# Kernel optimization log

Measured on AMD Instinct MI355X. Metric: run time of the kernel, lower is better.

Reference implementation:

```python
import jax, jax.numpy as jnp
import numpy as np

D_MODEL = 1024
D_INNER = 2048      # expand=2
D_STATE = 128
NHEADS = 32
HEADDIM = 64
DCONV = 4
CONV_DIM = D_INNER + 2 * D_STATE                 # x, B, C channels through conv
D_IN_PROJ = 2 * D_INNER + 2 * D_STATE + NHEADS   # z, xBC, dt
NBLOCKS = 4


def _mlp(x, w1, b1, w2, b2):
    # MLP(2, in, out): Linear(in,in) -> ReLU -> Linear(in,out)
    return jax.nn.relu(x @ w1 + b1) @ w2 + b2


def _mamba2_block(u, Wi, cw, cb, dtb, Alog, Dsk, nw, Wo):
    B, L, _ = u.shape
    zxbcdt = u @ Wi                                        # [B,L,D_IN_PROJ]
    z, xBC, dt = jnp.split(zxbcdt, [D_INNER, D_INNER + CONV_DIM], axis=-1)
    # causal depthwise conv1d, kernel 4
    pad = jnp.pad(xBC, ((0, 0), (DCONV - 1, 0), (0, 0)))
    conv = cb
    for k in range(DCONV):
        conv = conv + pad[:, k:k + L, :] * cw[:, k]
    xBC = jax.nn.silu(conv)
    xh, Bm, Cm = jnp.split(xBC, [D_INNER, D_INNER + D_STATE], axis=-1)
    dt = jax.nn.softplus(dt + dtb)                         # [B,L,H]
    A = -jnp.exp(Alog)                                     # [H], negative
    xh = xh.reshape(B, L, NHEADS, HEADDIM)

    def step(h, inp):
        x_t, dt_t, b_t, c_t = inp                          # [B,H,P],[B,H],[B,N],[B,N]
        dA = jnp.exp(dt_t * A)                             # [B,H]
        h = h * dA[..., None, None] + (dt_t[..., None] * x_t)[..., None] * b_t[:, None, None, :]
        y = jnp.einsum('bhpn,bn->bhp', h, c_t)
        return h, y

    h0 = jnp.zeros((B, NHEADS, HEADDIM, D_STATE), u.dtype)
    _, ys = jax.lax.scan(step, h0, (xh.transpose(1, 0, 2, 3), dt.transpose(1, 0, 2),
                                    Bm.transpose(1, 0, 2), Cm.transpose(1, 0, 2)))
    y = ys.transpose(1, 0, 2, 3) + Dsk[None, None, :, None] * xh   # D skip per head
    y = y.reshape(B, L, D_INNER)
    y = y * jax.nn.silu(z)                                 # gated RMSNorm (gate before norm)
    y = y * jax.lax.rsqrt(jnp.mean(y * y, axis=-1, keepdims=True) + 1e-5) * nw
    return y @ Wo


def setup_inputs() -> dict:
    key = jax.random.key(0)
    ks = jax.random.split(key, 16)
    B, S, STATE = 4, 512, 510
    s = 0.02
    return {
        'x': jax.random.normal(ks[0], (B, S, STATE), jnp.float32),
        'steps_left': jax.random.uniform(ks[1], (B, S, 1), jnp.float32) * 100.0,
        'current_r': jax.random.normal(ks[2], (B, S, 1), jnp.float32),
        'mlp_in_w1': jax.random.normal(ks[3], (STATE + 2, STATE + 2), jnp.float32) * s,
        'mlp_in_b1': jnp.zeros((STATE + 2,), jnp.float32),
        'mlp_in_w2': jax.random.normal(ks[4], (STATE + 2, D_MODEL), jnp.float32) * s,
        'mlp_in_b2': jnp.zeros((D_MODEL,), jnp.float32),
        'W_in': jax.random.normal(ks[5], (NBLOCKS, D_MODEL, D_IN_PROJ), jnp.float32) * s,
        'conv_w': jax.random.normal(ks[6], (NBLOCKS, CONV_DIM, DCONV), jnp.float32) * 0.2,
        'conv_b': jnp.zeros((NBLOCKS, CONV_DIM), jnp.float32),
        'dt_bias': jax.random.normal(ks[7], (NBLOCKS, NHEADS), jnp.float32) * 0.1,
        'A_log': jnp.log(jax.random.uniform(ks[8], (NBLOCKS, NHEADS), jnp.float32, 1.0, 16.0)),
        'D_skip': jnp.ones((NBLOCKS, NHEADS), jnp.float32),
        'norm_w': jnp.ones((NBLOCKS, D_INNER), jnp.float32),
        'W_out': jax.random.normal(ks[9], (NBLOCKS, D_INNER, D_MODEL), jnp.float32) * s,
        'mlp_out_w1': jax.random.normal(ks[10], (D_MODEL, D_MODEL), jnp.float32) * s,
        'mlp_out_b1': jnp.zeros((D_MODEL,), jnp.float32),
        'mlp_out_w2': jax.random.normal(ks[11], (D_MODEL, 1), jnp.float32) * s,
        'mlp_out_b2': jnp.zeros((1,), jnp.float32),
    }


def reference(x, steps_left, current_r,
              mlp_in_w1, mlp_in_b1, mlp_in_w2, mlp_in_b2,
              W_in, conv_w, conv_b, dt_bias, A_log, D_skip, norm_w, W_out,
              mlp_out_w1, mlp_out_b1, mlp_out_w2, mlp_out_b2):
    h = jnp.concatenate([x, steps_left, current_r], axis=-1)   # [B,S,state+2]
    h = _mlp(h, mlp_in_w1, mlp_in_b1, mlp_in_w2, mlp_in_b2)
    for i in range(NBLOCKS):
        h = _mamba2_block(h, W_in[i], conv_w[i], conv_b[i], dt_bias[i],
                          A_log[i], D_skip[i], norm_w[i], W_out[i])
    return _mlp(h, mlp_out_w1, mlp_out_b1, mlp_out_w2, mlp_out_b2)  # [B,S,1]
```

## Files before the change

kernel.cpp:

```cpp
#include <hip/hip_runtime.h>
#include <hip/hip_bf16.h>
#include <math.h>

#define D_MODEL   1024
#define D_INNER   2048
#define D_STATE   128
#define NHEADS    32
#define HEADDIM   64
#define DCONV     4
#define CONV_DIM  (D_INNER + 2 * D_STATE)
#define D_IN_PROJ (2 * D_INNER + 2 * D_STATE + NHEADS)
#define NBLOCKS   4
#define BATCH     4
#define SEQ       512
#define NTOK      (BATCH * SEQ)
#define STATE_IN  510
#define NPAD_IN   4480
#define NSEG      8
#define SEGLEN    64
#define NBH       (BATCH * NHEADS)
#define OFF_B     D_INNER
#define OFF_C     (D_INNER + D_STATE)
#define OFF_DT    (D_IN_PROJ - NHEADS)

typedef _Float16 half8_t __attribute__((ext_vector_type(8)));
typedef float f32x4_t  __attribute__((ext_vector_type(4)));
typedef unsigned short us;

__device__ __forceinline__ us f2h(float f) {
    _Float16 h = (_Float16)f;
    return __builtin_bit_cast(us, h);
}
__device__ __forceinline__ float h2f(us u) {
    return (float)__builtin_bit_cast(_Float16, u);
}
__device__ __forceinline__ void gl2lds16(const us* gp, us* lp) {
    __builtin_amdgcn_global_load_lds(
        (const __attribute__((address_space(1))) unsigned int*)(gp),
        (__attribute__((address_space(3))) unsigned int*)(lp), 16, 0, 0);
}

__global__ void concat_kernel(const float* __restrict__ x,
                              const float* __restrict__ steps,
                              const float* __restrict__ curr,
                              us* __restrict__ hcat)
{
    int idx = blockIdx.x * 256 + threadIdx.x;
    if (idx >= NTOK * 512) return;
    int bl = idx >> 9;
    int c  = idx & 511;
    float v;
    if (c < STATE_IN)       v = x[(size_t)bl * STATE_IN + c];
    else if (c == STATE_IN) v = steps[bl];
    else                    v = curr[bl];
    hcat[idx] = f2h(v);
}

__global__ __launch_bounds__(256)
void transpose_f16_kernel(const float* __restrict__ W, us* __restrict__ WT,
                          int K, int N)
{
    __shared__ us tile[32][36];
    int n0 = blockIdx.x * 32, k0 = blockIdx.y * 32;
    int t = threadIdx.x;
    int kl = t >> 3, nl = (t & 7) * 4;
    float4 v = make_float4(0.f, 0.f, 0.f, 0.f);
    if (n0 < N) v = *(const float4*)(W + (size_t)(k0 + kl) * N + n0 + nl);
    tile[nl + 0][kl] = f2h(v.x);
    tile[nl + 1][kl] = f2h(v.y);
    tile[nl + 2][kl] = f2h(v.z);
    tile[nl + 3][kl] = f2h(v.w);
    __syncthreads();
    int nl2 = t >> 3, kl2 = (t & 7) * 4;
    ushort4 o;
    o.x = tile[nl2][kl2 + 0];
    o.y = tile[nl2][kl2 + 1];
    o.z = tile[nl2][kl2 + 2];
    o.w = tile[nl2][kl2 + 3];
    *(ushort4*)(WT + (size_t)(n0 + nl2) * K + k0 + kl2) = o;
}

template<int BN, int TI>
__global__ __launch_bounds__(256)
void mfma_gemm_f16(const us* __restrict__ A, const us* __restrict__ BT,
                   const float* __restrict__ bias, us* __restrict__ C,
                   int N, int K, int relu)
{
    __shared__ us Al[128 * 32];
    __shared__ us Bl[BN * 32];
    const int tid = threadIdx.x, lane = tid & 63, wave = tid >> 6;
    const int g = lane >> 4, l16 = lane & 15;
    const int wr = (BN == 128) ? (wave >> 1) * 64 : wave * 32;
    const int wc = (BN == 128) ? (wave & 1) * 64 : 0;
    const int m0 = blockIdx.y * 128, n0 = blockIdx.x * BN;
    const int lrow = lane >> 2;
    const int lcol = ((lane & 3) ^ ((lrow >> 2) & 3)) * 8;

    f32x4_t acc[TI][4];
    const f32x4_t zero = {0.f, 0.f, 0.f, 0.f};
#pragma unroll
    for (int i = 0; i < TI; ++i)
#pragma unroll
        for (int j = 0; j < 4; ++j) acc[i][j] = zero;

    const us* abase = A  + (size_t)m0 * K;
    const us* bbase = BT + (size_t)n0 * K;

    for (int k0 = 0; k0 < K; k0 += 32) {
        __syncthreads();
#pragma unroll
        for (int s = 0; s < 2; ++s) {
            int rb = wave * 32 + s * 16;
            gl2lds16(abase + (size_t)(rb + lrow) * K + k0 + lcol, &Al[rb * 32]);
        }
#pragma unroll
        for (int s = 0; s < BN / 64; ++s) {
            int rb = wave * (BN / 4) + s * 16;
            gl2lds16(bbase + (size_t)(rb + lrow) * K + k0 + lcol, &Bl[rb * 32]);
        }
        __syncthreads();
        half8_t af[TI], bfr[4];
#pragma unroll
        for (int ti = 0; ti < TI; ++ti) {
            int r = wr + ti * 16 + l16;
            af[ti] = *(const half8_t*)&Al[r * 32 + ((g ^ ((r >> 2) & 3)) * 8)];
        }
#pragma unroll
        for (int tj = 0; tj < 4; ++tj) {
            int r = wc + tj * 16 + l16;
            bfr[tj] = *(const half8_t*)&Bl[r * 32 + ((g ^ ((r >> 2) & 3)) * 8)];
        }
#pragma unroll
        for (int ti = 0; ti < TI; ++ti)
#pragma unroll
            for (int tj = 0; tj < 4; ++tj)
                acc[ti][tj] = __builtin_amdgcn_mfma_f32_16x16x32_f16(
                    af[ti], bfr[tj], acc[ti][tj], 0, 0, 0);
    }

#pragma unroll
    for (int tj = 0; tj < 4; ++tj) {
        int col = n0 + wc + tj * 16 + l16;
        if (col >= N) continue;
        float bv = bias ? bias[col] : 0.f;
#pragma unroll
        for (int ti = 0; ti < TI; ++ti) {
            int rbase = m0 + wr + ti * 16 + g * 4;
#pragma unroll
            for (int r = 0; r < 4; ++r) {
                float v = acc[ti][tj][r] + bv;
                if (relu) v = fmaxf(v, 0.f);
                C[(size_t)(rbase + r) * N + col] = f2h(v);
            }
        }
    }
}

__global__ void conv_silu_kernel(const us* __restrict__ zxbcdt,
                                 const float* __restrict__ cw,
                                 const float* __restrict__ cb,
                                 us* __restrict__ xBCc)
{
    int idx = blockIdx.x * 256 + threadIdx.x;
    if (idx >= NTOK * CONV_DIM) return;
    int c  = idx % CONV_DIM;
    int bl = idx / CONV_DIM;
    int b  = bl >> 9;
    int l  = bl & 511;
    float acc = cb[c];
#pragma unroll
    for (int k = 0; k < DCONV; ++k) {
        int ll = l + k - (DCONV - 1);
        if (ll >= 0)
            acc = fmaf(h2f(zxbcdt[(size_t)(b * SEQ + ll) * D_IN_PROJ + D_INNER + c]),
                       cw[c * DCONV + k], acc);
    }
    xBCc[idx] = f2h(acc / (1.f + expf(-acc)));
}

__global__ __launch_bounds__(256)
void scan_seg_mfma_kernel(const us* __restrict__ zx, const us* __restrict__ xc,
                          const float* __restrict__ dt_bias,
                          const float* __restrict__ A_log,
                          const float* __restrict__ D_skip,
                          float* __restrict__ y, float* __restrict__ alpha,
                          us* __restrict__ Hseg)
{
    __shared__ __attribute__((aligned(16))) us Csh[64 * 128];
    __shared__ __attribute__((aligned(16))) us Bsh[64 * 128];
    __shared__ __attribute__((aligned(16))) us Bt[128 * 64];
    __shared__ __attribute__((aligned(16))) us Xt[64 * 64];
    __shared__ float dt_s[64], ls[64], csc[64];
    us* Ssh = Csh;
    const int bi = blockIdx.x, bh = bi >> 3, seg = bi & 7;
    const int b = bh >> 5, h = bh & 31;
    const int tid = threadIdx.x, lane = tid & 63, w = tid >> 6;
    const int g = lane >> 4, l16 = lane & 15;
    const int t0g = seg * SEGLEN;
    const size_t rowbase = (size_t)(b * SEQ + t0g);

    {
        int rr = lane >> 4, s = lane & 15;
#pragma unroll
        for (int it = 0; it < 4; ++it) {
            int rb = w * 16 + it * 4;
            int row = rb + rr;
            const us* src = xc + (rowbase + row) * CONV_DIM;
            int sw = (s ^ (row & 7)) * 8;
            gl2lds16(src + OFF_C + sw, &Csh[rb * 128]);
            gl2lds16(src + OFF_B + sw, &Bsh[rb * 128]);
        }
    }
#pragma unroll
    for (int qi = 0; qi < 4; ++qi) {
        int idx = tid + qi * 256;
        int pq = idx & 15, j = idx >> 4;
        ushort4 v = *(const ushort4*)(xc + (rowbase + j) * CONV_DIM + h * 64 + pq * 4);
#pragma unroll
        for (int e = 0; e < 4; ++e) {
            int p = pq * 4 + e;
            int pc = ((((j >> 3) ^ (p & 7)) << 3) | (j & 7));
            Xt[p * 64 + pc] = ((const us*)&v)[e];
        }
    }
#pragma unroll
    for (int qi = 0; qi < 8; ++qi) {
        int idx = tid + qi * 256;
        int nq = idx & 31, j = idx >> 5;
        ushort4 v = *(const ushort4*)(xc + (rowbase + j) * CONV_DIM + OFF_B + nq * 4);
#pragma unroll
        for (int e = 0; e < 4; ++e) {
            int n = nq * 4 + e;
            int pc = ((((j >> 3) ^ (n & 7)) << 3) | (j & 7));
            Bt[n * 64 + pc] = ((const us*)&v)[e];
        }
    }
    if (tid < 64) {
        int j = tid;
        float dtraw = h2f(zx[(rowbase + j) * D_IN_PROJ + OFF_DT + h]) + dt_bias[h];
        float dtv = (dtraw > 20.f) ? dtraw : log1pf(expf(dtraw));
        float ld = dtv * (-expf(A_log[h]));
#pragma unroll
        for (int o = 1; o < 64; o <<= 1) {
            float v = __shfl_up(ld, o);
            if (j >= o) ld += v;
        }
        float al = expf(ld);
        dt_s[j] = dtv;
        ls[j] = ld;
        alpha[(size_t)bh * SEQ + t0g + j] = al;
        float cend = __shfl(ld, 63);
        csc[j] = dtv * expf(cend - ld);
    }
    __syncthreads();

    const float Dsk = D_skip[h];
    const f32x4_t vzero = {0.f, 0.f, 0.f, 0.f};

    f32x4_t acc1[4];
#pragma unroll
    for (int jt = 0; jt < 4; ++jt) acc1[jt] = vzero;
    {
        int ia = w * 16 + l16;
#pragma unroll
        for (int ks = 0; ks < 4; ++ks) {
            half8_t a = *(const half8_t*)&Csh[ia * 128 + (((ks * 4 + g) ^ (ia & 7)) << 3)];
#pragma unroll
            for (int jt = 0; jt < 4; ++jt) {
                int jr = jt * 16 + l16;
                half8_t bfr = *(const half8_t*)&Bsh[jr * 128 + (((ks * 4 + g) ^ (jr & 7)) << 3)];
                acc1[jt] = __builtin_amdgcn_mfma_f32_16x16x32_f16(a, bfr, acc1[jt], 0, 0, 0);
            }
        }
    }
    __syncthreads();

    {
        int i0 = w * 16 + g * 4;
        float lsi[4];
#pragma unroll
        for (int r = 0; r < 4; ++r) lsi[r] = ls[i0 + r];
#pragma unroll
        for (int jt = 0; jt < 4; ++jt) {
            int j = jt * 16 + l16;
            float lj = ls[j], dj = dt_s[j];
#pragma unroll
            for (int r = 0; r < 4; ++r) {
                int i = i0 + r;
                float v = 0.f;
                if (j < i)       v = acc1[jt][r] * dj * expf(lsi[r] - lj);
                else if (j == i) v = acc1[jt][r] * dj + Dsk;
                int pc = ((((j >> 3) ^ (i & 7)) << 3) | (j & 7));
                Ssh[i * 64 + pc] = f2h(v);
            }
        }
    }
    __syncthreads();

    f32x4_t acc2[4];
#pragma unroll
    for (int nt = 0; nt < 4; ++nt) acc2[nt] = vzero;
    {
        int ia = w * 16 + l16;
#pragma unroll
        for (int ks = 0; ks < 2; ++ks) {
            half8_t a = *(const half8_t*)&Ssh[ia * 64 + (((ks * 4 + g) ^ (ia & 7)) << 3)];
#pragma unroll
            for (int nt = 0; nt < 4; ++nt) {
                int pr = nt * 16 + l16;
                half8_t bfr = *(const half8_t*)&Xt[pr * 64 + (((ks * 4 + g) ^ (pr & 7)) << 3)];
                acc2[nt] = __builtin_amdgcn_mfma_f32_16x16x32_f16(a, bfr, acc2[nt], 0, 0, 0);
            }
        }
    }
    {
        int i0 = w * 16 + g * 4;
#pragma unroll
        for (int nt = 0; nt < 4; ++nt) {
            int p = nt * 16 + l16;
#pragma unroll
            for (int r = 0; r < 4; ++r)
                y[(rowbase + i0 + r) * D_INNER + h * 64 + p] = acc2[nt][r];
        }
    }
    f32x4_t acc3[8];
#pragma unroll
    for (int nt = 0; nt < 8; ++nt) acc3[nt] = vzero;
    {
        int pa = w * 16 + l16;
#pragma unroll
        for (int ks = 0; ks < 2; ++ks) {
            half8_t araw = *(const half8_t*)&Xt[pa * 64 + (((ks * 4 + g) ^ (pa & 7)) << 3)];
            half8_t a;
#pragma unroll
            for (int e = 0; e < 8; ++e)
                a[e] = (_Float16)((float)araw[e] * csc[ks * 32 + g * 8 + e]);
#pragma unroll
            for (int nt = 0; nt < 8; ++nt) {
                int nr = nt * 16 + l16;
                half8_t bfr = *(const half8_t*)&Bt[nr * 64 + (((ks * 4 + g) ^ (nr & 7)) << 3)];
                acc3[nt] = __builtin_amdgcn_mfma_f32_16x16x32_f16(a, bfr, acc3[nt], 0, 0, 0);
            }
        }
    }
    {
        int p0 = w * 16 + g * 4;
#pragma unroll
        for (int nt = 0; nt < 8; ++nt) {
            int n = nt * 16 + l16;
#pragma unroll
            for (int r = 0; r < 4; ++r)
                Hseg[((size_t)bi * 64 + p0 + r) * 128 + n] = f2h(acc3[nt][r]);
        }
    }
}

__global__ __launch_bounds__(512)
void state_fixup_kernel(const float* __restrict__ alpha, us* __restrict__ Hseg)
{
    const int bh = blockIdx.x;
    const int t = threadIdx.x, p = t >> 3, ng = t & 7;
    float carry[16];
#pragma unroll
    for (int j = 0; j < 16; ++j) carry[j] = 0.f;
    for (int seg = 0; seg < NSEG; ++seg) {
        us* hs = Hseg + (((size_t)bh * NSEG + seg) * 64 + p) * 128;
        float ae = alpha[(size_t)bh * SEQ + seg * SEGLEN + SEGLEN - 1];
        float tmp[16];
#pragma unroll
        for (int q = 0; q < 4; ++q) {
            ushort4 u = *(const ushort4*)(hs + ng * 4 + q * 32);
            tmp[q*4+0] = h2f(u.x); tmp[q*4+1] = h2f(u.y);
            tmp[q*4+2] = h2f(u.z); tmp[q*4+3] = h2f(u.w);
        }
#pragma unroll
        for (int q = 0; q < 4; ++q) {
            ushort4 o;
            o.x = f2h(carry[q*4+0]); o.y = f2h(carry[q*4+1]);
            o.z = f2h(carry[q*4+2]); o.w = f2h(carry[q*4+3]);
            *(ushort4*)(hs + ng * 4 + q * 32) = o;
        }
#pragma unroll
        for (int j = 0; j < 16; ++j) carry[j] = fmaf(carry[j], ae, tmp[j]);
    }
}

__global__ __launch_bounds__(256)
void correct_mfma_kernel(const us* __restrict__ xc, const float* __restrict__ alpha,
                         const us* __restrict__ Hseg, float* __restrict__ y)
{
    __shared__ __attribute__((aligned(16))) us Csh[64 * 128];
    __shared__ __attribute__((aligned(16))) us Hsh[64 * 128];
    __shared__ float als_s[64];
    const int bi = blockIdx.x;
    const int bh = bi / 7, seg = 1 + (bi % 7);
    const int b = bh >> 5, h = bh & 31;
    const int tid = threadIdx.x, lane = tid & 63, w = tid >> 6;
    const int g = lane >> 4, l16 = lane & 15;
    const int t0g = seg * SEGLEN;
    const size_t rowbase = (size_t)(b * SEQ + t0g);
    const size_t hbase = (size_t)(bh * NSEG + seg) * 64;

    {
        int rr = lane >> 4, s = lane & 15;
#pragma unroll
        for (int it = 0; it < 4; ++it) {
            int rb = w * 16 + it * 4;
            int row = rb + rr;
            int sw = (s ^ (row & 7)) * 8;
            gl2lds16(xc + (rowbase + row) * CONV_DIM + OFF_C + sw, &Csh[rb * 128]);
            gl2lds16(Hseg + (hbase + row) * 128 + sw, &Hsh[rb * 128]);
        }
    }
    if (tid < 64) als_s[tid] = alpha[(size_t)bh * SEQ + t0g + tid];
    __syncthreads();

    const f32x4_t vzero = {0.f, 0.f, 0.f, 0.f};
    f32x4_t acc[4];
#pragma unroll
    for (int nt = 0; nt < 4; ++nt) acc[nt] = vzero;
    int ia = w * 16 + l16;
#pragma unroll
    for (int ks = 0; ks < 4; ++ks) {
        half8_t a = *(const half8_t*)&Csh[ia * 128 + (((ks * 4 + g) ^ (ia & 7)) << 3)];
#pragma unroll
        for (int nt = 0; nt < 4; ++nt) {
            int pr = nt * 16 + l16;
            half8_t bfr = *(const half8_t*)&Hsh[pr * 128 + (((ks * 4 + g) ^ (pr & 7)) << 3)];
            acc[nt] = __builtin_amdgcn_mfma_f32_16x16x32_f16(a, bfr, acc[nt], 0, 0, 0);
        }
    }
    int i0 = w * 16 + g * 4;
#pragma unroll
    for (int nt = 0; nt < 4; ++nt) {
        int p = nt * 16 + l16;
#pragma unroll
        for (int r = 0; r < 4; ++r) {
            size_t idx = (rowbase + i0 + r) * D_INNER + h * 64 + p;
            y[idx] += als_s[i0 + r] * acc[nt][r];
        }
    }
}

__global__ __launch_bounds__(256)
void gated_rmsnorm_kernel(const float* __restrict__ y,
                          const us* __restrict__ zxbcdt,
                          const float* __restrict__ norm_w,
                          us* __restrict__ yn)
{
    int bl = blockIdx.x;
    int t  = threadIdx.x;
    const float* yr = y + (size_t)bl * D_INNER;
    const us* zr = zxbcdt + (size_t)bl * D_IN_PROJ;
    us* outr = yn + (size_t)bl * D_INNER;

    float gv[8];
    float ss = 0.f;
#pragma unroll
    for (int q = 0; q < 8; ++q) {
        int j = t + q * 256;
        float z = h2f(zr[j]);
        float g = yr[j] * (z / (1.f + expf(-z)));
        gv[q] = g;
        ss += g * g;
    }
    __shared__ float red[256];
    red[t] = ss;
    __syncthreads();
    for (int w = 128; w > 0; w >>= 1) {
        if (t < w) red[t] += red[t + w];
        __syncthreads();
    }
    float rs = rsqrtf(red[0] / (float)D_INNER + 1e-5f);
#pragma unroll
    for (int q = 0; q < 8; ++q) {
        int j = t + q * 256;
        outr[j] = f2h(gv[q] * rs * norm_w[j]);
    }
}

__global__ __launch_bounds__(256)
void final_dot_kernel(const us* __restrict__ t1,
                      const float* __restrict__ w2,
                      const float* __restrict__ b2,
                      float* __restrict__ out)
{
    int bl = blockIdx.x;
    int t  = threadIdx.x;
    float s = 0.f;
    for (int j = t; j < D_MODEL; j += 256)
        s = fmaf(h2f(t1[(size_t)bl * D_MODEL + j]), w2[j], s);
    __shared__ float red[256];
    red[t] = s;
    __syncthreads();
    for (int w = 128; w > 0; w >>= 1) {
        if (t < w) red[t] += red[t + w];
        __syncthreads();
    }
    if (t == 0) out[bl] = red[0] + b2[0];
}

extern "C" void kernel_launch(void* const* d_in, const int* in_sizes, int n_in,
                              void* d_out, int out_size, void* d_ws, size_t ws_size,
                              hipStream_t stream)
{
    const float* x        = (const float*)d_in[0];
    const float* steps    = (const float*)d_in[1];
    const float* curr     = (const float*)d_in[2];
    const float* mi_w1    = (const float*)d_in[3];
    const float* mi_b1    = (const float*)d_in[4];
    const float* mi_w2    = (const float*)d_in[5];
    const float* mi_b2    = (const float*)d_in[6];
    const float* W_in     = (const float*)d_in[7];
    const float* conv_w   = (const float*)d_in[8];
    const float* conv_b   = (const float*)d_in[9];
    const float* dt_bias  = (const float*)d_in[10];
    const float* A_log    = (const float*)d_in[11];
    const float* D_skip   = (const float*)d_in[12];
    const float* norm_w   = (const float*)d_in[13];
    const float* W_out    = (const float*)d_in[14];
    const float* mo_w1    = (const float*)d_in[15];
    const float* mo_b1    = (const float*)d_in[16];
    const float* mo_w2    = (const float*)d_in[17];
    const float* mo_b2    = (const float*)d_in[18];
    float* out = (float*)d_out;

    us* wt_mi1 = (us*)d_ws;
    us* wt_mi2 = wt_mi1 + (size_t)512 * 512;
    us* wt_in  = wt_mi2 + (size_t)1024 * 512;
    us* wt_out = wt_in  + (size_t)4 * NPAD_IN * 1024;
    us* wt_mo1 = wt_out + (size_t)4 * 1024 * 2048;
    us* Hseg   = wt_mo1 + (size_t)1024 * 1024;
    us* hcat   = Hseg   + (size_t)NBH * NSEG * 64 * 128;
    us* h      = hcat   + (size_t)NTOK * 512;
    us* zxb    = h      + (size_t)NTOK * D_MODEL;
    us* xc     = zxb    + (size_t)NTOK * D_IN_PROJ;
    us* yn     = xc     + (size_t)NTOK * CONV_DIM;
    us* t0     = zxb;
    us* t1     = xc;
    float* fbase = (float*)((((uintptr_t)(yn + (size_t)NTOK * D_INNER)) + 255)
                            & ~(uintptr_t)255);
    float* y     = fbase;
    float* alpha = y + (size_t)NTOK * D_INNER;

    transpose_f16_kernel<<<dim3(512/32, 512/32), 256, 0, stream>>>(mi_w1, wt_mi1, 512, 512);
    transpose_f16_kernel<<<dim3(1024/32, 512/32), 256, 0, stream>>>(mi_w2, wt_mi2, 512, 1024);
    for (int i = 0; i < NBLOCKS; ++i) {
        transpose_f16_kernel<<<dim3(NPAD_IN/32, 1024/32), 256, 0, stream>>>(
            W_in + (size_t)i * D_MODEL * D_IN_PROJ, wt_in + (size_t)i * NPAD_IN * 1024,
            D_MODEL, D_IN_PROJ);
        transpose_f16_kernel<<<dim3(1024/32, 2048/32), 256, 0, stream>>>(
            W_out + (size_t)i * D_INNER * D_MODEL, wt_out + (size_t)i * 1024 * 2048,
            D_INNER, D_MODEL);
    }
    transpose_f16_kernel<<<dim3(1024/32, 1024/32), 256, 0, stream>>>(mo_w1, wt_mo1, 1024, 1024);

    concat_kernel<<<(NTOK * 512 + 255) / 256, 256, 0, stream>>>(x, steps, curr, hcat);

    mfma_gemm_f16<64, 2><<<dim3(512/64, NTOK/128), 256, 0, stream>>>(
        hcat, wt_mi1, mi_b1, t0, 512, 512, 1);
    mfma_gemm_f16<64, 2><<<dim3(1024/64, NTOK/128), 256, 0, stream>>>(
        t0, wt_mi2, mi_b2, h, 1024, 512, 0);

    for (int i = 0; i < NBLOCKS; ++i) {
        mfma_gemm_f16<128, 4><<<dim3(NPAD_IN/128, NTOK/128), 256, 0, stream>>>(
            h, wt_in + (size_t)i * NPAD_IN * 1024, nullptr, zxb, D_IN_PROJ, D_MODEL, 0);
        conv_silu_kernel<<<(NTOK * CONV_DIM + 255) / 256, 256, 0, stream>>>(
            zxb, conv_w + (size_t)i * CONV_DIM * DCONV, conv_b + (size_t)i * CONV_DIM, xc);
        scan_seg_mfma_kernel<<<NBH * NSEG, 256, 0, stream>>>(
            zxb, xc, dt_bias + i * NHEADS, A_log + i * NHEADS, D_skip + i * NHEADS,
            y, alpha, Hseg);
        state_fixup_kernel<<<NBH, 512, 0, stream>>>(alpha, Hseg);
        correct_mfma_kernel<<<NBH * (NSEG - 1), 256, 0, stream>>>(xc, alpha, Hseg, y);
        gated_rmsnorm_kernel<<<NTOK, 256, 0, stream>>>(
            y, zxb, norm_w + (size_t)i * D_INNER, yn);
        mfma_gemm_f16<64, 2><<<dim3(1024/64, NTOK/128), 256, 0, stream>>>(
            yn, wt_out + (size_t)i * 1024 * 2048, nullptr, h, 1024, 2048, 0);
    }

    mfma_gemm_f16<64, 2><<<dim3(1024/64, NTOK/128), 256, 0, stream>>>(
        h, wt_mo1, mo_b1, t1, 1024, 1024, 1);
    final_dot_kernel<<<NTOK, 256, 0, stream>>>(t1, mo_w2, mo_b2, out);
}
```

Baseline: 813.8 us.

## Triple-buffer LDS tiles in MFMA GEMM with async global-to-LDS prefetch

Turns the single-buffered GEMM K loop into a three-stage pipeline. Tiles for k+2 are issued into a rotating LDS buffer while the current tile is consumed. Explicit vmcnt waits plus one barrier per iteration replace the two __syncthreads, so global load latency can overlap with the MFMA work. LDS use triples, which may lower occupancy, and the hand-set vmcnt counts must match the number of loads issued per stage.

```diff
diff --git a/kernel.cpp b/kernel.cpp
--- a/kernel.cpp
+++ b/kernel.cpp
@@ -86,8 +86,8 @@
                    const float* __restrict__ bias, us* __restrict__ C,
                    int N, int K, int relu)
 {
-    __shared__ us Al[128 * 32];
-    __shared__ us Bl[BN * 32];
+    __shared__ __attribute__((aligned(16))) us Al[3][128 * 32];
+    __shared__ __attribute__((aligned(16))) us Bl[3][BN * 32];
     const int tid = threadIdx.x, lane = tid & 63, wave = tid >> 6;
     const int g = lane >> 4, l16 = lane & 15;
     const int wr = (BN == 128) ? (wave >> 1) * 64 : wave * 32;
@@ -106,29 +106,48 @@
     const us* abase = A  + (size_t)m0 * K;
     const us* bbase = BT + (size_t)n0 * K;
 
-    for (int k0 = 0; k0 < K; k0 += 32) {
-        __syncthreads();
+    auto stage = [&](int buf, int k0) {
 #pragma unroll
         for (int s = 0; s < 2; ++s) {
             int rb = wave * 32 + s * 16;
-            gl2lds16(abase + (size_t)(rb + lrow) * K + k0 + lcol, &Al[rb * 32]);
+            gl2lds16(abase + (size_t)(rb + lrow) * K + k0 + lcol, &Al[buf][rb * 32]);
         }
 #pragma unroll
         for (int s = 0; s < BN / 64; ++s) {
             int rb = wave * (BN / 4) + s * 16;
-            gl2lds16(bbase + (size_t)(rb + lrow) * K + k0 + lcol, &Bl[rb * 32]);
-        }
-        __syncthreads();
+            gl2lds16(bbase + (size_t)(rb + lrow) * K + k0 + lcol, &Bl[buf][rb * 32]);
+        }
+    };
+
+    const int NT = K >> 5;
+    stage(0, 0);
+    stage(1, 32);
+
+    int cur = 0;
+    for (int t = 0; t < NT; ++t) {
+        if (t == NT - 1) {
+            asm volatile("s_waitcnt vmcnt(0)" ::: "memory");
+        } else if constexpr (BN == 128) {
+            asm volatile("s_waitcnt vmcnt(4)" ::: "memory");
+        } else {
+            asm volatile("s_waitcnt vmcnt(3)" ::: "memory");
+        }
+        __builtin_amdgcn_s_barrier();
+        if (t + 2 < NT) {
+            int s2 = cur + 2; if (s2 >= 3) s2 -= 3;
+            stage(s2, (t + 2) << 5);
+        }
+
         half8_t af[TI], bfr[4];
 #pragma unroll
         for (int ti = 0; ti < TI; ++ti) {
             int r = wr + ti * 16 + l16;
-            af[ti] = *(const half8_t*)&Al[r * 32 + ((g ^ ((r >> 2) & 3)) * 8)];
+            af[ti] = *(const half8_t*)&Al[cur][r * 32 + ((g ^ ((r >> 2) & 3)) * 8)];
         }
 #pragma unroll
         for (int tj = 0; tj < 4; ++tj) {
             int r = wc + tj * 16 + l16;
-            bfr[tj] = *(const half8_t*)&Bl[r * 32 + ((g ^ ((r >> 2) & 3)) * 8)];
+            bfr[tj] = *(const half8_t*)&Bl[cur][r * 32 + ((g ^ ((r >> 2) & 3)) * 8)];
         }
 #pragma unroll
         for (int ti = 0; ti < TI; ++ti)
@@ -136,6 +155,8 @@
             for (int tj = 0; tj < 4; ++tj)
                 acc[ti][tj] = __builtin_amdgcn_mfma_f32_16x16x32_f16(
                     af[ti], bfr[tj], acc[ti][tj], 0, 0, 0);
+
+        cur = (cur == 2) ? 0 : cur + 1;
     }
 
 #pragma unroll
```

Measured after the change: 787.8 us. 1.03x faster.
